# Optimization experiments

Hardware: AMD Instinct MI355X
Metric: run time of the kernel (lower is better)

Reference implementation:

```python
import jax, jax.numpy as jnp
import numpy as np

B, T, D = 64, 2048, 512
H = 512  # max(64, d_model)
G, S, A = 4, 6, 4
TAU = 0.5
EPS = 1e-5


def setup_inputs() -> dict:
    key = jax.random.key(0)
    ks = jax.random.split(key, 24)
    sc = 0.02
    inp = {
        "x": jax.random.normal(ks[0], (B, T, D), jnp.float32),
        # global_net: Linear(D,H) -> LayerNorm(H) -> GELU -> Linear(H,G)
        "gW1": jax.random.normal(ks[1], (D, H), jnp.float32) * sc,
        "gb1": jnp.zeros((H,), jnp.float32),
        "g_ln_w": jnp.ones((H,), jnp.float32),
        "g_ln_b": jnp.zeros((H,), jnp.float32),
        "gW2": jax.random.normal(ks[2], (H, G), jnp.float32) * sc,
        "gb2": jnp.zeros((G,), jnp.float32),
        # sector_net: Linear(D,H) -> GELU -> Linear(H, D*S)
        "sW1": jax.random.normal(ks[3], (D, H), jnp.float32) * sc,
        "sb1": jnp.zeros((H,), jnp.float32),
        "sW2": jax.random.normal(ks[4], (H, D * S), jnp.float32) * sc,
        "sb2": jnp.zeros((D * S,), jnp.float32),
        # asset_net: Linear(D,H) -> GELU -> Linear(H, D*A)
        "aW1": jax.random.normal(ks[5], (D, H), jnp.float32) * sc,
        "ab1": jnp.zeros((H,), jnp.float32),
        "aW2": jax.random.normal(ks[6], (H, D * A), jnp.float32) * sc,
        "ab2": jnp.zeros((D * A,), jnp.float32),
        # priors
        "g_prior": jnp.zeros((G,), jnp.float32),
        "s_prior": jnp.zeros((S,), jnp.float32),
        "a_prior": jnp.zeros((A,), jnp.float32),
        # global_to_feature: Linear(G, D, bias=False), stored as (G, D)
        "g2f_W": jax.random.normal(ks[7], (G, D), jnp.float32) * sc,
        "sec_emb": jax.random.normal(ks[8], (S, D), jnp.float32),
        "ast_emb": jax.random.normal(ks[9], (A, D), jnp.float32),
    }
    return inp


def _layernorm(h, w, b):
    m = h.mean(-1, keepdims=True)
    v = ((h - m) ** 2).mean(-1, keepdims=True)
    return (h - m) * jax.lax.rsqrt(v + EPS) * w + b


def _gumbel_softmax(logits, key):
    g = jax.random.gumbel(key, logits.shape, logits.dtype)
    return jax.nn.softmax((logits + g) / TAU, axis=-1)


def _kl_categorical(post_logits, prior_logits):
    log_p = jax.nn.log_softmax(post_logits, axis=-1)
    log_q = jax.nn.log_softmax(prior_logits, axis=-1)
    return jnp.sum(jnp.exp(log_p) * (log_p - log_q), axis=-1)


def reference(x, gW1, gb1, g_ln_w, g_ln_b, gW2, gb2,
              sW1, sb1, sW2, sb2, aW1, ab1, aW2, ab2,
              g_prior, s_prior, a_prior, g2f_W, sec_emb, ast_emb):
    b, _, f = x.shape  # f == D
    seq_mean = x.mean(axis=1)                       # (B, D)
    diff_summary = (x[:, 1:, :] - x[:, :-1, :]).mean(axis=1)  # (B, D)

    g_h = _layernorm(seq_mean @ gW1 + gb1, g_ln_w, g_ln_b)
    global_logits = jax.nn.gelu(g_h, approximate=False) @ gW2 + gb2  # (B, G)

    s_h = jax.nn.gelu(seq_mean @ sW1 + sb1, approximate=False)
    sector_logits = (s_h @ sW2 + sb2).reshape(b, f, S)   # (B, D, S)

    a_h = jax.nn.gelu(diff_summary @ aW1 + ab1, approximate=False)
    asset_logits = (a_h @ aW2 + ab2).reshape(b, f, A)    # (B, D, A)

    gk = jax.random.split(jax.random.key(42), 3)
    global_probs = _gumbel_softmax(global_logits, gk[0])
    sector_probs = _gumbel_softmax(sector_logits, gk[1])
    asset_probs = _gumbel_softmax(asset_logits, gk[2])

    kl_global = _kl_categorical(global_logits, g_prior).mean()
    kl_sector = _kl_categorical(sector_logits, s_prior).mean()
    kl_asset = _kl_categorical(asset_logits, a_prior).mean()

    global_gate = global_probs @ g2f_W                         # (B, D)
    # einsum-then-diagonal fused: diag[b,f] = sum_s probs[b,f,s] * emb[s,f]
    sector_gate = jnp.einsum('bfs,sf->bf', sector_probs, sec_emb)
    asset_gate = jnp.einsum('bfs,sf->bf', asset_probs, ast_emb)
    feature_gate = jax.nn.sigmoid(global_gate + sector_gate + asset_gate)

    return (global_probs, sector_probs, asset_probs, feature_gate,
            kl_global, kl_sector, kl_asset)
```

## Files before the change

### kernel.cpp

```cpp
#include <hip/hip_runtime.h>


#define NB 64
#define NT 2048
#define ND 512
#define NH 512
#define NG 4
#define NS 6
#define NA 4

typedef unsigned int u32;

struct TF2 { u32 a, b; };

__host__ __device__ constexpr u32 rotl32(u32 x, int r) { return (x << r) | (x >> (32 - r)); }

__host__ __device__ constexpr TF2 tf2x32(u32 k0, u32 k1, u32 x0, u32 x1) {
  u32 ks2 = k0 ^ k1 ^ 0x1BD11BDAu;
  x0 += k0; x1 += k1;
  x0 += x1; x1 = rotl32(x1, 13); x1 ^= x0;
  x0 += x1; x1 = rotl32(x1, 15); x1 ^= x0;
  x0 += x1; x1 = rotl32(x1, 26); x1 ^= x0;
  x0 += x1; x1 = rotl32(x1, 6);  x1 ^= x0;
  x0 += k1;  x1 += ks2 + 1u;
  x0 += x1; x1 = rotl32(x1, 17); x1 ^= x0;
  x0 += x1; x1 = rotl32(x1, 29); x1 ^= x0;
  x0 += x1; x1 = rotl32(x1, 16); x1 ^= x0;
  x0 += x1; x1 = rotl32(x1, 24); x1 ^= x0;
  x0 += ks2; x1 += k0 + 2u;
  x0 += x1; x1 = rotl32(x1, 13); x1 ^= x0;
  x0 += x1; x1 = rotl32(x1, 15); x1 ^= x0;
  x0 += x1; x1 = rotl32(x1, 26); x1 ^= x0;
  x0 += x1; x1 = rotl32(x1, 6);  x1 ^= x0;
  x0 += k0;  x1 += k1 + 3u;
  x0 += x1; x1 = rotl32(x1, 17); x1 ^= x0;
  x0 += x1; x1 = rotl32(x1, 29); x1 ^= x0;
  x0 += x1; x1 = rotl32(x1, 16); x1 ^= x0;
  x0 += x1; x1 = rotl32(x1, 24); x1 ^= x0;
  x0 += k1;  x1 += ks2 + 4u;
  x0 += x1; x1 = rotl32(x1, 13); x1 ^= x0;
  x0 += x1; x1 = rotl32(x1, 15); x1 ^= x0;
  x0 += x1; x1 = rotl32(x1, 26); x1 ^= x0;
  x0 += x1; x1 = rotl32(x1, 6);  x1 ^= x0;
  x0 += ks2; x1 += k0 + 5u;
  return TF2{x0, x1};
}

constexpr TF2 GKG = tf2x32(0u, 42u, 0u, 0u);
constexpr TF2 GKS = tf2x32(0u, 42u, 0u, 1u);
constexpr TF2 GKA = tf2x32(0u, 42u, 0u, 2u);

__device__ inline float gumbel32(u32 k0, u32 k1, u32 idx) {
  TF2 r = tf2x32(k0, k1, 0u, idx);
  u32 bits = r.a ^ r.b;
  float f = __uint_as_float((bits >> 9) | 0x3f800000u) - 1.0f;
  f = fmaxf(f, 1.17549435e-38f);
  return -logf(-logf(f));
}

__device__ inline float gelu_exact(float x) {
  return 0.5f * x * (1.0f + erff(x * 0.70710678118654752f));
}

__global__ __launch_bounds__(256) void k_partial(const float* __restrict__ x,
                                                 float* __restrict__ part,
                                                 float* __restrict__ klacc) {
  if (blockIdx.x == 0 && threadIdx.x < 3) klacc[threadIdx.x] = 0.0f;
  int bx = blockIdx.x;
  int b = bx >> 4, c = bx & 15;
  int tid = threadIdx.x;
  int q = tid & 127;
  int rg = tid >> 7;
  const float* base = x + ((size_t)(b * NT + c * 128 + rg) * ND + q * 4);
  float4 acc = make_float4(0.f, 0.f, 0.f, 0.f);
#pragma unroll 8
  for (int i = 0; i < 64; ++i) {
    float4 v = *reinterpret_cast<const float4*>(base + (size_t)i * 2 * ND);
    acc.x += v.x; acc.y += v.y; acc.z += v.z; acc.w += v.w;
  }
  __shared__ float sm[2][ND];
  *reinterpret_cast<float4*>(&sm[rg][q * 4]) = acc;
  __syncthreads();
  float* p = part + (size_t)bx * ND;
  p[tid]       = sm[0][tid] + sm[1][tid];
  p[tid + 256] = sm[0][tid + 256] + sm[1][tid + 256];
}

__global__ __launch_bounds__(256) void k_means(const float* __restrict__ part,
                                               const float* __restrict__ x,
                                               float* __restrict__ seq,
                                               float* __restrict__ diff) {
  int b = blockIdx.x, tid = threadIdx.x;
  int d = tid * 2;
  float2 s = make_float2(0.f, 0.f);
  const float* p = part + (size_t)b * 16 * ND + d;
#pragma unroll
  for (int c = 0; c < 16; ++c) {
    float2 v = *reinterpret_cast<const float2*>(p + (size_t)c * ND);
    s.x += v.x; s.y += v.y;
  }
  seq[b * ND + d]     = s.x * (1.0f / (float)NT);
  seq[b * ND + d + 1] = s.y * (1.0f / (float)NT);
  const float* x0 = x + (size_t)b * NT * ND;
  const float* xl = x0 + (size_t)(NT - 1) * ND;
  const float inv = 1.0f / (float)(NT - 1);
  diff[b * ND + d]     = (xl[d]     - x0[d])     * inv;
  diff[b * ND + d + 1] = (xl[d + 1] - x0[d + 1]) * inv;
}

__global__ __launch_bounds__(256) void k_gemm1(
    const float* __restrict__ seq, const float* __restrict__ diff,
    const float* __restrict__ gW1, const float* __restrict__ gb1,
    const float* __restrict__ sW1, const float* __restrict__ sb1,
    const float* __restrict__ aW1, const float* __restrict__ ab1,
    float* __restrict__ pre) {
  int bx = blockIdx.x;
  int mu = bx >> 6; int rem = bx & 63;
  int m0 = (rem >> 3) * 8, n0 = (rem & 7) * 64;
  const float* Asrc = (mu == 2) ? diff : seq;
  const float* W = (mu == 0) ? gW1 : (mu == 1) ? sW1 : aW1;
  const float* bias = (mu == 0) ? gb1 : (mu == 1) ? sb1 : ab1;
  __shared__ float As[8][ND];
  int tid = threadIdx.x;
  for (int r = 0; r < 16; ++r) {
    int idx = r * 256 + tid;
    As[idx >> 9][idx & 511] = Asrc[(size_t)(m0 + (idx >> 9)) * ND + (idx & 511)];
  }
  __syncthreads();
  int n = n0 + (tid & 63);
  int ml = (tid >> 6) * 2;
  float a0 = 0.f, a1 = 0.f;
#pragma unroll 8
  for (int k = 0; k < ND; ++k) {
    float w = W[(size_t)k * NH + n];
    a0 += As[ml][k] * w;
    a1 += As[ml + 1][k] * w;
  }
  float bb = bias[n];
  pre[(size_t)(m0 + ml) * 1536 + mu * 512 + n]     = a0 + bb;
  pre[(size_t)(m0 + ml + 1) * 1536 + mu * 512 + n] = a1 + bb;
}

__global__ __launch_bounds__(256) void k_act(const float* __restrict__ pre,
                                             const float* __restrict__ lnw,
                                             const float* __restrict__ lnb,
                                             float* __restrict__ act) {
  int b = blockIdx.x, tid = threadIdx.x;
  const float* p = pre + (size_t)b * 1536;
  float* a = act + (size_t)b * 1536;
  __shared__ float red[8];
  float v0 = p[tid], v1 = p[tid + 256];
  float s = v0 + v1;
#pragma unroll
  for (int o = 32; o > 0; o >>= 1) s += __shfl_down(s, o, 64);
  int wid = tid >> 6, lane = tid & 63;
  if (lane == 0) red[wid] = s;
  __syncthreads();
  if (tid == 0) red[0] = (red[0] + red[1] + red[2] + red[3]) * (1.0f / 512.0f);
  __syncthreads();
  float mean = red[0];
  float d0 = v0 - mean, d1 = v1 - mean;
  float q = d0 * d0 + d1 * d1;
#pragma unroll
  for (int o = 32; o > 0; o >>= 1) q += __shfl_down(q, o, 64);
  if (lane == 0) red[4 + wid] = q;
  __syncthreads();
  if (tid == 0) red[1] = (red[4] + red[5] + red[6] + red[7]) * (1.0f / 512.0f);
  __syncthreads();
  float r = 1.0f / sqrtf(red[1] + 1e-5f);
  float h0 = d0 * r * lnw[tid] + lnb[tid];
  float h1 = d1 * r * lnw[tid + 256] + lnb[tid + 256];
  a[tid] = gelu_exact(h0);
  a[tid + 256] = gelu_exact(h1);
#pragma unroll
  for (int j = 0; j < 4; ++j) {
    int idx = 512 + j * 256 + tid;
    a[idx] = gelu_exact(p[idx]);
  }
}

__global__ __launch_bounds__(256) void k_gemm2(
    const float* __restrict__ act,
    const float* __restrict__ gW2, const float* __restrict__ gb2,
    const float* __restrict__ sW2, const float* __restrict__ sb2,
    const float* __restrict__ aW2, const float* __restrict__ ab2,
    float* __restrict__ lg, float* __restrict__ ls, float* __restrict__ la) {
  int bx = blockIdx.x;
  int mt = bx / 81, j = bx % 81;
  int mu, n0, N; const float *W, *bias; float* out; int ld;
  if (j == 0)       { mu = 0; n0 = 0;             N = NG;   W = gW2; bias = gb2; out = lg; ld = NG; }
  else if (j <= 48) { mu = 1; n0 = (j - 1) * 64;  N = 3072; W = sW2; bias = sb2; out = ls; ld = 3072; }
  else              { mu = 2; n0 = (j - 49) * 64; N = 2048; W = aW2; bias = ab2; out = la; ld = 2048; }
  int m0 = mt * 8;
  __shared__ float As[8][NH];
  int tid = threadIdx.x;
  for (int r = 0; r < 16; ++r) {
    int idx = r * 256 + tid;
    As[idx >> 9][idx & 511] = act[(size_t)(m0 + (idx >> 9)) * 1536 + mu * 512 + (idx & 511)];
  }
  __syncthreads();
  int nl = tid & 63;
  int ml = (tid >> 6) * 2;
  if (nl < N) {
    int n = n0 + nl;
    float a0 = 0.f, a1 = 0.f;
#pragma unroll 8
    for (int k = 0; k < NH; ++k) {
      float w = W[(size_t)k * N + n];
      a0 += As[ml][k] * w;
      a1 += As[ml + 1][k] * w;
    }
    float bb = bias[n];
    out[(size_t)(m0 + ml) * ld + n]     = a0 + bb;
    out[(size_t)(m0 + ml + 1) * ld + n] = a1 + bb;
  }
}

__global__ __launch_bounds__(128) void k_final(
    const float* __restrict__ lg, const float* __restrict__ ls,
    const float* __restrict__ la,
    const float* __restrict__ g_prior, const float* __restrict__ s_prior,
    const float* __restrict__ a_prior, const float* __restrict__ g2f,
    const float* __restrict__ semb, const float* __restrict__ aemb,
    float* __restrict__ out, float* __restrict__ klacc) {
  int bx = blockIdx.x;
  int b = bx >> 2, fq = bx & 3;
  int tid = threadIdx.x;
  __shared__ float gp[NG];
  if (tid == 0) {
    float l[NG], z[NG];
    float zm = -1e30f;
#pragma unroll
    for (int g = 0; g < NG; ++g) {
      l[g] = lg[b * NG + g];
      float gn = gumbel32(GKG.a, GKG.b, (u32)(b * NG + g));
      z[g] = (l[g] + gn) * 2.0f;
      zm = fmaxf(zm, z[g]);
    }
    float zs = 0.f;
#pragma unroll
    for (int g = 0; g < NG; ++g) { z[g] = expf(z[g] - zm); zs += z[g]; }
    float inv = 1.0f / zs;
#pragma unroll
    for (int g = 0; g < NG; ++g) gp[g] = z[g] * inv;
    if (fq == 0) {
#pragma unroll
      for (int g = 0; g < NG; ++g) out[b * NG + g] = gp[g];
      float lm = -1e30f, qm = -1e30f, q[NG];
#pragma unroll
      for (int g = 0; g < NG; ++g) {
        q[g] = g_prior[g];
        lm = fmaxf(lm, l[g]); qm = fmaxf(qm, q[g]);
      }
      float le = 0.f, qe = 0.f;
#pragma unroll
      for (int g = 0; g < NG; ++g) { le += expf(l[g] - lm); qe += expf(q[g] - qm); }
      float lls = logf(le), qls = logf(qe);
      float kl = 0.f;
#pragma unroll
      for (int g = 0; g < NG; ++g) {
        float lp = l[g] - lm - lls, lq = q[g] - qm - qls;
        kl += expf(lp) * (lp - lq);
      }
      atomicAdd(&klacc[0], kl);
    }
  }
  __syncthreads();
  int f = fq * 128 + tid;

  float sl[NS], sz[NS], sp[NS];
  u32 sbase = (u32)((b * ND + f) * NS);
  const float* lsp = ls + (size_t)b * 3072 + f * NS;
  float zm = -1e30f;
#pragma unroll
  for (int s = 0; s < NS; ++s) {
    sl[s] = lsp[s];
    float gn = gumbel32(GKS.a, GKS.b, sbase + s);
    sz[s] = (sl[s] + gn) * 2.0f;
    zm = fmaxf(zm, sz[s]);
  }
  float zs = 0.f;
#pragma unroll
  for (int s = 0; s < NS; ++s) { sz[s] = expf(sz[s] - zm); zs += sz[s]; }
  float inv = 1.0f / zs;
  float* outs = out + 256 + (size_t)sbase;
#pragma unroll
  for (int s = 0; s < NS; ++s) { sp[s] = sz[s] * inv; outs[s] = sp[s]; }
  float lm = -1e30f;
#pragma unroll
  for (int s = 0; s < NS; ++s) lm = fmaxf(lm, sl[s]);
  float le = 0.f;
#pragma unroll
  for (int s = 0; s < NS; ++s) le += expf(sl[s] - lm);
  float lls = logf(le);
  float q6[NS], qm = -1e30f;
#pragma unroll
  for (int s = 0; s < NS; ++s) { q6[s] = s_prior[s]; qm = fmaxf(qm, q6[s]); }
  float qe = 0.f;
#pragma unroll
  for (int s = 0; s < NS; ++s) qe += expf(q6[s] - qm);
  float qls = logf(qe);
  float klS = 0.f;
#pragma unroll
  for (int s = 0; s < NS; ++s) {
    float lp = sl[s] - lm - lls, lq = q6[s] - qm - qls;
    klS += expf(lp) * (lp - lq);
  }

  float al[NA], az[NA], ap[NA];
  u32 abase = (u32)((b * ND + f) * NA);
  const float* lap = la + (size_t)b * 2048 + f * NA;
  zm = -1e30f;
#pragma unroll
  for (int a = 0; a < NA; ++a) {
    al[a] = lap[a];
    float gn = gumbel32(GKA.a, GKA.b, abase + a);
    az[a] = (al[a] + gn) * 2.0f;
    zm = fmaxf(zm, az[a]);
  }
  zs = 0.f;
#pragma unroll
  for (int a = 0; a < NA; ++a) { az[a] = expf(az[a] - zm); zs += az[a]; }
  inv = 1.0f / zs;
  float* outa = out + 196864 + (size_t)abase;
#pragma unroll
  for (int a = 0; a < NA; ++a) { ap[a] = az[a] * inv; outa[a] = ap[a]; }
  lm = -1e30f;
#pragma unroll
  for (int a = 0; a < NA; ++a) lm = fmaxf(lm, al[a]);
  le = 0.f;
#pragma unroll
  for (int a = 0; a < NA; ++a) le += expf(al[a] - lm);
  lls = logf(le);
  float q4[NA]; qm = -1e30f;
#pragma unroll
  for (int a = 0; a < NA; ++a) { q4[a] = a_prior[a]; qm = fmaxf(qm, q4[a]); }
  qe = 0.f;
#pragma unroll
  for (int a = 0; a < NA; ++a) qe += expf(q4[a] - qm);
  qls = logf(qe);
  float klA = 0.f;
#pragma unroll
  for (int a = 0; a < NA; ++a) {
    float lp = al[a] - lm - lls, lq = q4[a] - qm - qls;
    klA += expf(lp) * (lp - lq);
  }

  float gg = 0.f;
#pragma unroll
  for (int g = 0; g < NG; ++g) gg += gp[g] * g2f[g * ND + f];
  float sg = 0.f;
#pragma unroll
  for (int s = 0; s < NS; ++s) sg += sp[s] * semb[s * ND + f];
  float ag = 0.f;
#pragma unroll
  for (int a = 0; a < NA; ++a) ag += ap[a] * aemb[a * ND + f];
  float xg = gg + sg + ag;
  out[327936 + b * ND + f] = 1.0f / (1.0f + expf(-xg));

#pragma unroll
  for (int o = 32; o > 0; o >>= 1) {
    klS += __shfl_down(klS, o, 64);
    klA += __shfl_down(klA, o, 64);
  }
  if ((tid & 63) == 0) {
    atomicAdd(&klacc[1], klS);
    atomicAdd(&klacc[2], klA);
  }
}

__global__ void k_scalars(const float* __restrict__ klacc, float* __restrict__ out) {
  if (threadIdx.x == 0 && blockIdx.x == 0) {
    out[360704] = klacc[0] * (1.0f / 64.0f);
    out[360705] = klacc[1] * (1.0f / 32768.0f);
    out[360706] = klacc[2] * (1.0f / 32768.0f);
  }
}

extern "C" void kernel_launch(void* const* d_in, const int* in_sizes, int n_in,
                              void* d_out, int out_size, void* d_ws, size_t ws_size,
                              hipStream_t stream) {
  const float* x       = (const float*)d_in[0];
  const float* gW1     = (const float*)d_in[1];
  const float* gb1     = (const float*)d_in[2];
  const float* g_ln_w  = (const float*)d_in[3];
  const float* g_ln_b  = (const float*)d_in[4];
  const float* gW2     = (const float*)d_in[5];
  const float* gb2     = (const float*)d_in[6];
  const float* sW1     = (const float*)d_in[7];
  const float* sb1     = (const float*)d_in[8];
  const float* sW2     = (const float*)d_in[9];
  const float* sb2     = (const float*)d_in[10];
  const float* aW1     = (const float*)d_in[11];
  const float* ab1     = (const float*)d_in[12];
  const float* aW2     = (const float*)d_in[13];
  const float* ab2     = (const float*)d_in[14];
  const float* g_prior = (const float*)d_in[15];
  const float* s_prior = (const float*)d_in[16];
  const float* a_prior = (const float*)d_in[17];
  const float* g2f     = (const float*)d_in[18];
  const float* semb    = (const float*)d_in[19];
  const float* aemb    = (const float*)d_in[20];

  float* ws   = (float*)d_ws;
  float* part = ws;
  float* seq  = part + 524288;
  float* diff = seq + 32768;
  float* pre  = diff + 32768;
  float* act  = pre + 98304;
  float* lg   = act + 98304;
  float* ls   = lg + 256;
  float* la   = ls + 196608;
  float* klacc = la + 131072;

  float* out = (float*)d_out;

  hipLaunchKernelGGL(k_partial, dim3(1024), dim3(256), 0, stream, x, part, klacc);
  hipLaunchKernelGGL(k_means,   dim3(64),   dim3(256), 0, stream, part, x, seq, diff);
  hipLaunchKernelGGL(k_gemm1,   dim3(192),  dim3(256), 0, stream,
                     seq, diff, gW1, gb1, sW1, sb1, aW1, ab1, pre);
  hipLaunchKernelGGL(k_act,     dim3(64),   dim3(256), 0, stream, pre, g_ln_w, g_ln_b, act);
  hipLaunchKernelGGL(k_gemm2,   dim3(648),  dim3(256), 0, stream,
                     act, gW2, gb2, sW2, sb2, aW2, ab2, lg, ls, la);
  hipLaunchKernelGGL(k_final,   dim3(256),  dim3(128), 0, stream,
                     lg, ls, la, g_prior, s_prior, a_prior, g2f, semb, aemb, out, klacc);
  hipLaunchKernelGGL(k_scalars, dim3(1),    dim3(64),  0, stream, klacc, out);
}
```

Before: 492.9 us.

## Fuse mean/GEMM1/activation kernels, widen GEMM2 tiles, fold scalar finalize into last block

```diff
diff --git a/kernel.cpp b/kernel.cpp
--- a/kernel.cpp
+++ b/kernel.cpp
@@ -62,19 +62,19 @@
   return 0.5f * x * (1.0f + erff(x * 0.70710678118654752f));
 }
 
-__global__ __launch_bounds__(256) void k_partial(const float* __restrict__ x,
-                                                 float* __restrict__ part,
-                                                 float* __restrict__ klacc) {
-  if (blockIdx.x == 0 && threadIdx.x < 3) klacc[threadIdx.x] = 0.0f;
+__global__ __launch_bounds__(256, 8) void k_partial(const float* __restrict__ x,
+                                                    float* __restrict__ part,
+                                                    float* __restrict__ klacc) {
+  if (blockIdx.x == 0 && threadIdx.x < 4) klacc[threadIdx.x] = 0.0f;
   int bx = blockIdx.x;
-  int b = bx >> 4, c = bx & 15;
+  int b = bx >> 5, c = bx & 31;
   int tid = threadIdx.x;
   int q = tid & 127;
   int rg = tid >> 7;
-  const float* base = x + ((size_t)(b * NT + c * 128 + rg) * ND + q * 4);
+  const float* base = x + ((size_t)(b * NT + c * 64 + rg) * ND + q * 4);
   float4 acc = make_float4(0.f, 0.f, 0.f, 0.f);
 #pragma unroll 8
-  for (int i = 0; i < 64; ++i) {
+  for (int i = 0; i < 32; ++i) {
     float4 v = *reinterpret_cast<const float4*>(base + (size_t)i * 2 * ND);
     acc.x += v.x; acc.y += v.y; acc.z += v.z; acc.w += v.w;
   }
@@ -86,96 +86,109 @@
   p[tid + 256] = sm[0][tid + 256] + sm[1][tid + 256];
 }
 
-__global__ __launch_bounds__(256) void k_means(const float* __restrict__ part,
-                                               const float* __restrict__ x,
-                                               float* __restrict__ seq,
-                                               float* __restrict__ diff) {
-  int b = blockIdx.x, tid = threadIdx.x;
-  int d = tid * 2;
-  float2 s = make_float2(0.f, 0.f);
-  const float* p = part + (size_t)b * 16 * ND + d;
-#pragma unroll
-  for (int c = 0; c < 16; ++c) {
-    float2 v = *reinterpret_cast<const float2*>(p + (size_t)c * ND);
-    s.x += v.x; s.y += v.y;
-  }
-  seq[b * ND + d]     = s.x * (1.0f / (float)NT);
-  seq[b * ND + d + 1] = s.y * (1.0f / (float)NT);
-  const float* x0 = x + (size_t)b * NT * ND;
-  const float* xl = x0 + (size_t)(NT - 1) * ND;
-  const float inv = 1.0f / (float)(NT - 1);
-  diff[b * ND + d]     = (xl[d]     - x0[d])     * inv;
-  diff[b * ND + d + 1] = (xl[d + 1] - x0[d + 1]) * inv;
-}
-
-__global__ __launch_bounds__(256) void k_gemm1(
-    const float* __restrict__ seq, const float* __restrict__ diff,
+__global__ __launch_bounds__(256) void k_gemm1act(
+    const float* __restrict__ part, const float* __restrict__ x,
     const float* __restrict__ gW1, const float* __restrict__ gb1,
+    const float* __restrict__ g_ln_w, const float* __restrict__ g_ln_b,
     const float* __restrict__ sW1, const float* __restrict__ sb1,
     const float* __restrict__ aW1, const float* __restrict__ ab1,
-    float* __restrict__ pre) {
+    float* __restrict__ act) {
   int bx = blockIdx.x;
-  int mu = bx >> 6; int rem = bx & 63;
-  int m0 = (rem >> 3) * 8, n0 = (rem & 7) * 64;
-  const float* Asrc = (mu == 2) ? diff : seq;
-  const float* W = (mu == 0) ? gW1 : (mu == 1) ? sW1 : aW1;
+  int mu = bx >> 5;
+  int m0 = (bx & 31) * 2;
+  const float* W    = (mu == 0) ? gW1 : (mu == 1) ? sW1 : aW1;
   const float* bias = (mu == 0) ? gb1 : (mu == 1) ? sb1 : ab1;
-  __shared__ float As[8][ND];
   int tid = threadIdx.x;
-  for (int r = 0; r < 16; ++r) {
-    int idx = r * 256 + tid;
-    As[idx >> 9][idx & 511] = Asrc[(size_t)(m0 + (idx >> 9)) * ND + (idx & 511)];
+  int colp = tid * 2;
+
+  __shared__ float2 As[ND];
+  if (mu < 2) {
+    const float* p0 = part + (size_t)m0 * 32 * ND + colp;
+    const float* p1 = part + (size_t)(m0 + 1) * 32 * ND + colp;
+    float2 s0 = make_float2(0.f, 0.f), s1 = make_float2(0.f, 0.f);
+#pragma unroll 8
+    for (int c = 0; c < 32; ++c) {
+      float2 v0 = *reinterpret_cast<const float2*>(p0 + (size_t)c * ND);
+      float2 v1 = *reinterpret_cast<const float2*>(p1 + (size_t)c * ND);
+      s0.x += v0.x; s0.y += v0.y; s1.x += v1.x; s1.y += v1.y;
+    }
+    const float inv = 1.0f / (float)NT;
+    As[colp]     = make_float2(s0.x * inv, s1.x * inv);
+    As[colp + 1] = make_float2(s0.y * inv, s1.y * inv);
+  } else {
+    const float inv = 1.0f / (float)(NT - 1);
+    const float* xr0 = x + (size_t)m0 * NT * ND + colp;
+    const float* xr1 = x + (size_t)(m0 + 1) * NT * ND + colp;
+    float2 f0 = *reinterpret_cast<const float2*>(xr0);
+    float2 l0 = *reinterpret_cast<const float2*>(xr0 + (size_t)(NT - 1) * ND);
+    float2 f1 = *reinterpret_cast<const float2*>(xr1);
+    float2 l1 = *reinterpret_cast<const float2*>(xr1 + (size_t)(NT - 1) * ND);
+    As[colp]     = make_float2((l0.x - f0.x) * inv, (l1.x - f1.x) * inv);
+    As[colp + 1] = make_float2((l0.y - f0.y) * inv, (l1.y - f1.y) * inv);
   }
   __syncthreads();
-  int n = n0 + (tid & 63);
-  int ml = (tid >> 6) * 2;
-  float a0 = 0.f, a1 = 0.f;
+
+  float2 acc0 = make_float2(0.f, 0.f), acc1 = make_float2(0.f, 0.f);
 #pragma unroll 8
   for (int k = 0; k < ND; ++k) {
-    float w = W[(size_t)k * NH + n];
-    a0 += As[ml][k] * w;
-    a1 += As[ml + 1][k] * w;
-  }
-  float bb = bias[n];
-  pre[(size_t)(m0 + ml) * 1536 + mu * 512 + n]     = a0 + bb;
-  pre[(size_t)(m0 + ml + 1) * 1536 + mu * 512 + n] = a1 + bb;
-}
-
-__global__ __launch_bounds__(256) void k_act(const float* __restrict__ pre,
-                                             const float* __restrict__ lnw,
-                                             const float* __restrict__ lnb,
-                                             float* __restrict__ act) {
-  int b = blockIdx.x, tid = threadIdx.x;
-  const float* p = pre + (size_t)b * 1536;
-  float* a = act + (size_t)b * 1536;
-  __shared__ float red[8];
-  float v0 = p[tid], v1 = p[tid + 256];
-  float s = v0 + v1;
-#pragma unroll
-  for (int o = 32; o > 0; o >>= 1) s += __shfl_down(s, o, 64);
-  int wid = tid >> 6, lane = tid & 63;
-  if (lane == 0) red[wid] = s;
-  __syncthreads();
-  if (tid == 0) red[0] = (red[0] + red[1] + red[2] + red[3]) * (1.0f / 512.0f);
-  __syncthreads();
-  float mean = red[0];
-  float d0 = v0 - mean, d1 = v1 - mean;
-  float q = d0 * d0 + d1 * d1;
-#pragma unroll
-  for (int o = 32; o > 0; o >>= 1) q += __shfl_down(q, o, 64);
-  if (lane == 0) red[4 + wid] = q;
-  __syncthreads();
-  if (tid == 0) red[1] = (red[4] + red[5] + red[6] + red[7]) * (1.0f / 512.0f);
-  __syncthreads();
-  float r = 1.0f / sqrtf(red[1] + 1e-5f);
-  float h0 = d0 * r * lnw[tid] + lnb[tid];
-  float h1 = d1 * r * lnw[tid + 256] + lnb[tid + 256];
-  a[tid] = gelu_exact(h0);
-  a[tid + 256] = gelu_exact(h1);
-#pragma unroll
-  for (int j = 0; j < 4; ++j) {
-    int idx = 512 + j * 256 + tid;
-    a[idx] = gelu_exact(p[idx]);
+    float2 wv = *reinterpret_cast<const float2*>(&W[(size_t)k * NH + colp]);
+    float2 a = As[k];
+    acc0.x += a.x * wv.x; acc0.y += a.x * wv.y;
+    acc1.x += a.y * wv.x; acc1.y += a.y * wv.y;
+  }
+  float2 bb = *reinterpret_cast<const float2*>(&bias[colp]);
+  acc0.x += bb.x; acc0.y += bb.y;
+  acc1.x += bb.x; acc1.y += bb.y;
+
+  float* arow0 = act + (size_t)m0 * 1536 + mu * 512;
+  float* arow1 = act + (size_t)(m0 + 1) * 1536 + mu * 512;
+
+  if (mu == 0) {
+    __shared__ float red[2][4];
+    __shared__ float mv[4];
+    int wid = tid >> 6, lane = tid & 63;
+    float s0 = acc0.x + acc0.y, s1 = acc1.x + acc1.y;
+#pragma unroll
+    for (int o = 32; o > 0; o >>= 1) {
+      s0 += __shfl_down(s0, o, 64);
+      s1 += __shfl_down(s1, o, 64);
+    }
+    if (lane == 0) { red[0][wid] = s0; red[1][wid] = s1; }
+    __syncthreads();
+    if (tid == 0) {
+      mv[0] = (red[0][0] + red[0][1] + red[0][2] + red[0][3]) * (1.0f / 512.0f);
+      mv[1] = (red[1][0] + red[1][1] + red[1][2] + red[1][3]) * (1.0f / 512.0f);
+    }
+    __syncthreads();
+    float m0v = mv[0], m1v = mv[1];
+    float d0x = acc0.x - m0v, d0y = acc0.y - m0v;
+    float d1x = acc1.x - m1v, d1y = acc1.y - m1v;
+    float q0 = d0x * d0x + d0y * d0y, q1 = d1x * d1x + d1y * d1y;
+#pragma unroll
+    for (int o = 32; o > 0; o >>= 1) {
+      q0 += __shfl_down(q0, o, 64);
+      q1 += __shfl_down(q1, o, 64);
+    }
+    if (lane == 0) { red[0][wid] = q0; red[1][wid] = q1; }
+    __syncthreads();
+    if (tid == 0) {
+      mv[2] = (red[0][0] + red[0][1] + red[0][2] + red[0][3]) * (1.0f / 512.0f);
+      mv[3] = (red[1][0] + red[1][1] + red[1][2] + red[1][3]) * (1.0f / 512.0f);
+    }
+    __syncthreads();
+    float r0 = 1.0f / sqrtf(mv[2] + 1e-5f);
+    float r1 = 1.0f / sqrtf(mv[3] + 1e-5f);
+    float2 lw = *reinterpret_cast<const float2*>(&g_ln_w[colp]);
+    float2 lb = *reinterpret_cast<const float2*>(&g_ln_b[colp]);
+    arow0[colp]     = gelu_exact(d0x * r0 * lw.x + lb.x);
+    arow0[colp + 1] = gelu_exact(d0y * r0 * lw.y + lb.y);
+    arow1[colp]     = gelu_exact(d1x * r1 * lw.x + lb.x);
+    arow1[colp + 1] = gelu_exact(d1y * r1 * lw.y + lb.y);
+  } else {
+    arow0[colp]     = gelu_exact(acc0.x);
+    arow0[colp + 1] = gelu_exact(acc0.y);
+    arow1[colp]     = gelu_exact(acc1.x);
+    arow1[colp + 1] = gelu_exact(acc1.y);
   }
 }
 
@@ -186,11 +199,11 @@
     const float* __restrict__ aW2, const float* __restrict__ ab2,
     float* __restrict__ lg, float* __restrict__ ls, float* __restrict__ la) {
   int bx = blockIdx.x;
-  int mt = bx / 81, j = bx % 81;
-  int mu, n0, N; const float *W, *bias; float* out; int ld;
-  if (j == 0)       { mu = 0; n0 = 0;             N = NG;   W = gW2; bias = gb2; out = lg; ld = NG; }
-  else if (j <= 48) { mu = 1; n0 = (j - 1) * 64;  N = 3072; W = sW2; bias = sb2; out = ls; ld = 3072; }
-  else              { mu = 2; n0 = (j - 49) * 64; N = 2048; W = aW2; bias = ab2; out = la; ld = 2048; }
+  int mt = bx / 41, j = bx % 41;
+  int mu, n0, N; const float *W, *bias; float* out;
+  if (j == 0)       { mu = 0; n0 = 0;              N = NG;   W = gW2; bias = gb2; out = lg; }
+  else if (j <= 24) { mu = 1; n0 = (j - 1) * 128;  N = 3072; W = sW2; bias = sb2; out = ls; }
+  else              { mu = 2; n0 = (j - 25) * 128; N = 2048; W = aW2; bias = ab2; out = la; }
   int m0 = mt * 8;
   __shared__ float As[8][NH];
   int tid = threadIdx.x;
@@ -199,20 +212,23 @@
     As[idx >> 9][idx & 511] = act[(size_t)(m0 + (idx >> 9)) * 1536 + mu * 512 + (idx & 511)];
   }
   __syncthreads();
-  int nl = tid & 63;
+  int nl = (tid & 63) * 2;
   int ml = (tid >> 6) * 2;
   if (nl < N) {
     int n = n0 + nl;
-    float a0 = 0.f, a1 = 0.f;
+    float2 a0 = make_float2(0.f, 0.f), a1 = make_float2(0.f, 0.f);
 #pragma unroll 8
     for (int k = 0; k < NH; ++k) {
-      float w = W[(size_t)k * N + n];
-      a0 += As[ml][k] * w;
-      a1 += As[ml + 1][k] * w;
-    }
-    float bb = bias[n];
-    out[(size_t)(m0 + ml) * ld + n]     = a0 + bb;
-    out[(size_t)(m0 + ml + 1) * ld + n] = a1 + bb;
+      float2 w = *reinterpret_cast<const float2*>(&W[(size_t)k * N + n]);
+      float s0 = As[ml][k], s1 = As[ml + 1][k];
+      a0.x += s0 * w.x; a0.y += s0 * w.y;
+      a1.x += s1 * w.x; a1.y += s1 * w.y;
+    }
+    float2 bb = *reinterpret_cast<const float2*>(&bias[n]);
+    a0.x += bb.x; a0.y += bb.y;
+    a1.x += bb.x; a1.y += bb.y;
+    *reinterpret_cast<float2*>(&out[(size_t)(m0 + ml) * N + n])     = a0;
+    *reinterpret_cast<float2*>(&out[(size_t)(m0 + ml + 1) * N + n]) = a1;
   }
 }
 
@@ -367,13 +383,20 @@
     atomicAdd(&klacc[1], klS);
     atomicAdd(&klacc[2], klA);
   }
-}
-
-__global__ void k_scalars(const float* __restrict__ klacc, float* __restrict__ out) {
-  if (threadIdx.x == 0 && blockIdx.x == 0) {
-    out[360704] = klacc[0] * (1.0f / 64.0f);
-    out[360705] = klacc[1] * (1.0f / 32768.0f);
-    out[360706] = klacc[2] * (1.0f / 32768.0f);
+
+  __syncthreads();
+  __threadfence();
+  if (tid == 0) {
+    u32 old = atomicAdd(reinterpret_cast<u32*>(&klacc[3]), 1u);
+    if (old == 255u) {
+      __threadfence();
+      float kg  = atomicAdd(&klacc[0], 0.0f);
+      float ksv = atomicAdd(&klacc[1], 0.0f);
+      float kav = atomicAdd(&klacc[2], 0.0f);
+      out[360704] = kg  * (1.0f / 64.0f);
+      out[360705] = ksv * (1.0f / 32768.0f);
+      out[360706] = kav * (1.0f / 32768.0f);
+    }
   }
 }
 
@@ -402,27 +425,21 @@
   const float* semb    = (const float*)d_in[19];
   const float* aemb    = (const float*)d_in[20];
 
-  float* ws   = (float*)d_ws;
-  float* part = ws;
-  float* seq  = part + 524288;
-  float* diff = seq + 32768;
-  float* pre  = diff + 32768;
-  float* act  = pre + 98304;
-  float* lg   = act + 98304;
-  float* ls   = lg + 256;
-  float* la   = ls + 196608;
+  float* ws    = (float*)d_ws;
+  float* part  = ws;
+  float* act   = part + 1048576;
+  float* lg    = act + 98304;
+  float* ls    = lg + 256;
+  float* la    = ls + 196608;
   float* klacc = la + 131072;
 
   float* out = (float*)d_out;
 
-  hipLaunchKernelGGL(k_partial, dim3(1024), dim3(256), 0, stream, x, part, klacc);
-  hipLaunchKernelGGL(k_means,   dim3(64),   dim3(256), 0, stream, part, x, seq, diff);
-  hipLaunchKernelGGL(k_gemm1,   dim3(192),  dim3(256), 0, stream,
-                     seq, diff, gW1, gb1, sW1, sb1, aW1, ab1, pre);
-  hipLaunchKernelGGL(k_act,     dim3(64),   dim3(256), 0, stream, pre, g_ln_w, g_ln_b, act);
-  hipLaunchKernelGGL(k_gemm2,   dim3(648),  dim3(256), 0, stream,
+  hipLaunchKernelGGL(k_partial,  dim3(2048), dim3(256), 0, stream, x, part, klacc);
+  hipLaunchKernelGGL(k_gemm1act, dim3(96),   dim3(256), 0, stream,
+                     part, x, gW1, gb1, g_ln_w, g_ln_b, sW1, sb1, aW1, ab1, act);
+  hipLaunchKernelGGL(k_gemm2,    dim3(328),  dim3(256), 0, stream,
                      act, gW2, gb2, sW2, sb2, aW2, ab2, lg, ls, la);
-  hipLaunchKernelGGL(k_final,   dim3(256),  dim3(128), 0, stream,
+  hipLaunchKernelGGL(k_final,    dim3(256),  dim3(128), 0, stream,
                      lg, ls, la, g_prior, s_prior, a_prior, g2f, semb, aemb, out, klacc);
-  hipLaunchKernelGGL(k_scalars, dim3(1),    dim3(64),  0, stream, klacc, out);
-}
+}
```

Measured after the change: 502.7 us. No clear change (+2.0%).
